# Kernel optimization log

Hardware: AMD Instinct MI355X
Metric: run time of the kernel (lower is better)

The kernel has to match this reference:

```python
import jax, jax.numpy as jnp
import numpy as np
from jax import lax

A = 20          # alphabet size (input_size)
L = 512         # max_seq_length
CH = 8          # conv channels
N_LAYERS = 9    # log2(512) conv+pool stages


def setup_inputs() -> dict:
    key = jax.random.key(0)
    ks = jax.random.split(key, 6)
    B = 1024
    idx = jax.random.randint(ks[0], (B, L), 0, A)
    lens = jax.random.randint(ks[1], (B,), L // 4, L + 1)
    masks = jnp.arange(L)[None, :] < lens[:, None]            # [B, L] bool
    # one-hot sequences, zeroed at padded positions (so nonzero() skips them)
    x = jax.nn.one_hot(idx, A, dtype=jnp.float32) * masks[..., None].astype(jnp.float32)
    blosum = jax.random.normal(ks[2], (A, A), jnp.float32)
    blosum = (blosum + blosum.T) * 0.5                        # symmetric like BLOSUM
    lpm = blosum                                              # trainable copy
    pm = jnp.clip(blosum, 0.0)                                # clamp(min=0) constant
    std = jnp.ones((1,), jnp.float32)                         # Gaussian std for row decay
    w0 = jax.random.normal(ks[3], (CH, 1, 3), jnp.float32) * 0.3
    ws = jax.random.normal(ks[4], (N_LAYERS - 1, CH, CH, 3), jnp.float32) * 0.2
    return {"x": x, "masks": masks, "lpm": lpm, "pm": pm, "std": std, "w0": w0, "ws": ws}


def _shift_pos(m, k):
    # target index clamp(s + k, max=L-1): shift right by k, boundary index L-1
    # collects any source in the last k+1 positions (set semantics -> OR).
    head = jnp.zeros(m.shape[:-1] + (k,), dtype=bool)
    body = m[..., : L - k - 1]                                # targets k .. L-2
    last = jnp.any(m[..., L - 1 - k:], axis=-1, keepdims=True)
    return jnp.concatenate([head, body, last], axis=-1)


def _shift_neg(m, k):
    # target index clamp(s - k, min=0)
    first = jnp.any(m[..., : k + 1], axis=-1, keepdims=True)
    body = m[..., k + 1:]                                     # targets 1 .. L-1-k
    tail = jnp.zeros(m.shape[:-1] + (k,), dtype=bool)
    return jnp.concatenate([first, body, tail], axis=-1)


def _column(nz, lpm, pm):
    # Banded substitution scatter: each one-hot row i writes V[i, r] into row r
    # at the same (batch, seq) position. Original nested index_put loops collapse
    # to a single 20x20 matrix V applied via einsum (one-hot => no collisions).
    ii = jnp.arange(A)[:, None]
    rr = jnp.arange(A)[None, :]
    M = jnp.clip(lpm, 0.001, 1.0) * pm
    # up-writes: j in 1..18-i => i < r <= 18 ; down-writes: j in 1..i => r < i
    V = jnp.where((rr > ii) & (rr <= A - 2), M, 0.0) + jnp.where(rr < ii, M.T, 0.0)
    return jnp.einsum('bis,ir->brs', nz, V)


def _row(m, std):
    # Gaussian positional decay: writes exp(-k^2/(2 std^2)) at seq offsets +-k,
    # k = 1,2,3 in order (later k overwrites earlier at clamp collisions).
    row = jnp.zeros(m.shape, jnp.float32)
    for k in (1, 2, 3):
        mk = _shift_pos(m, k) | _shift_neg(m, k)
        vk = jnp.exp(-(k * k) / (2.0 * std * std))[0]
        row = jnp.where(mk, vk, row)
    return row


def _conv1d(h, w):
    # Conv1d(kernel=3, stride=1, pad=1, no bias)
    return lax.conv_general_dilated(h, w, (1,), [(1, 1)],
                                    dimension_numbers=('NCH', 'OIH', 'NCH'))


def _avgpool2(h):
    N, C, Lh = h.shape
    return h.reshape(N, C, Lh // 2, 2).mean(-1)


def reference(x, masks, lpm, pm, std, w0, ws):
    B = x.shape[0]
    xp = jnp.transpose(x, (0, 2, 1))          # [B, 20, L]
    m = xp != 0
    nz = m.astype(xp.dtype)
    h = xp + _column(nz, lpm, pm) + _row(m, std)
    h = h.reshape(B * A, 1, L)
    h = _avgpool2(_conv1d(h, w0))
    for i in range(N_LAYERS - 1):
        h = _avgpool2(_conv1d(h, ws[i]))
    return h.squeeze(-1).reshape(B, A, -1)    # [B, 20, 8]
```

## Files before the change

kernel.cpp:

```cpp
#include <hip/hip_runtime.h>
#include <math.h>

#define LSEQ 512
#define NA 20
#define NCH 8
#define SV 33
#define PSTRIDE 168

__global__ __launch_bounds__(256) void wf_vt_kernel(
    const float* __restrict__ w0,
    const float* __restrict__ wsg,
    const float* __restrict__ lpm,
    const float* __restrict__ pm,
    float* __restrict__ wf,
    float* __restrict__ vtn)
{
    const int t = threadIdx.x;

    if (blockIdx.x == NCH) {
        for (int o = t; o < NA * NA; o += 256) {
            int j = o / NA, a = o % NA;
            float v = 0.f;
            if (a > j && a <= NA - 2)
                v += fminf(fmaxf(lpm[j * NA + a], 0.001f), 1.0f) * pm[j * NA + a];
            if (a < j)
                v += fminf(fmaxf(lpm[a * NA + j], 0.001f), 1.0f) * pm[a * NA + j];
            vtn[o] = v;
        }
        return;
    }

    const int r = blockIdx.x;

    __shared__ float gA[NCH * 256];
    __shared__ float gB[NCH * 256];
    __shared__ float4 s_e[NCH * NCH];

    if (t < NCH) gA[t * 256] = (t == r) ? 1.f : 0.f;
    __syncthreads();

    int P = 1;
    for (int step = 0; step < 8; ++step) {
        const int li = 7 - step;
        if (t < 64) {
            const int co = t >> 3, ci = t & 7;
            const float* wp = wsg + li * 192 + co * 24 + ci * 3;
            const float a0 = wp[0], a1 = wp[1], a2 = wp[2];
            s_e[co * 8 + ci] = make_float4(a0 + a1, a2, a1 + a2, a0);
        }
        __syncthreads();
        const float* gi = (step & 1) ? gB : gA;
        float* go = (step & 1) ? gA : gB;
        for (int it = t; it < NCH * P; it += 256) {
            const int ci = it >> step;
            const int p = it & (P - 1);
            float accE = 0.f, accO = 0.f;
#pragma unroll
            for (int co = 0; co < NCH; ++co) {
                const float g0 = gi[co * 256 + p];
                const float gm = (p > 0) ? gi[co * 256 + p - 1] : 0.f;
                const float gp = (p + 1 < P) ? gi[co * 256 + p + 1] : 0.f;
                const float4 e = s_e[co * 8 + ci];
                accE += e.x * g0 + e.y * gm;
                accO += e.z * g0 + e.w * gp;
            }
            *(float2*)(go + ci * 256 + 2 * p) = make_float2(0.5f * accE, 0.5f * accO);
        }
        __syncthreads();
        P <<= 1;
    }

    {
        const int p = t;
        float accE = 0.f, accO = 0.f;
#pragma unroll
        for (int co = 0; co < NCH; ++co) {
            const float g0 = gA[co * 256 + p];
            const float gm = (p > 0) ? gA[co * 256 + p - 1] : 0.f;
            const float gp = (p < 255) ? gA[co * 256 + p + 1] : 0.f;
            const float q0 = w0[co * 3 + 0], q1 = w0[co * 3 + 1], q2 = w0[co * 3 + 2];
            accE += (q0 + q1) * g0 + q2 * gm;
            accO += (q1 + q2) * g0 + q0 * gp;
        }
        *(float2*)(wf + r * 512 + 2 * p) = make_float2(0.5f * accE, 0.5f * accO);
    }
}

#define BUILD_H(S_)                                                                     \
    do {                                                                                \
        const int s = (S_);                                                             \
        const int ai = s_idx[s];                                                        \
        const bool valid = ai < NA;                                                     \
        _Pragma("unroll")                                                               \
        for (int a = 0; a < NA; ++a) {                                                  \
            float v = valid ? (s_vtn[ai * SV + a] + (a == ai ? 1.f : 0.f)) : 0.f;       \
            s_h[a * 256 + t] = v;                                                       \
        }                                                                               \
        _Pragma("unroll")                                                               \
        for (int k = 1; k <= 3; ++k) {                                                  \
            const float add = (k == 1) ? vk1 : (k == 2) ? vk2 : vk3;                    \
            if (s == LSEQ - 1) {                                                        \
                for (int u = LSEQ - 1 - k; u <= LSEQ - 1; ++u) {                        \
                    int tg = s_idx[u];                                                  \
                    if (tg < NA)                                                        \
                        s_h[tg * 256 + t] =                                             \
                            (valid ? s_vtn[ai * SV + tg] + (tg == ai ? 1.f : 0.f) : 0.f) + add; \
                }                                                                       \
            } else if (s >= k) {                                                        \
                int tg = s_idx[s - k];                                                  \
                if (tg < NA)                                                            \
                    s_h[tg * 256 + t] =                                                 \
                        (valid ? s_vtn[ai * SV + tg] + (tg == ai ? 1.f : 0.f) : 0.f) + add; \
            }                                                                           \
            if (s == 0) {                                                               \
                for (int u = 0; u <= k; ++u) {                                          \
                    int tg = s_idx[u];                                                  \
                    if (tg < NA)                                                        \
                        s_h[tg * 256 + t] =                                             \
                            (valid ? s_vtn[ai * SV + tg] + (tg == ai ? 1.f : 0.f) : 0.f) + add; \
                }                                                                       \
            } else if (s + k < LSEQ) {                                                  \
                int tg = s_idx[s + k];                                                  \
                if (tg < NA)                                                            \
                    s_h[tg * 256 + t] =                                                 \
                        (valid ? s_vtn[ai * SV + tg] + (tg == ai ? 1.f : 0.f) : 0.f) + add; \
            }                                                                           \
        }                                                                               \
    } while (0)

#define DOT_ROW(J_, ACC_)                                                               \
    do {                                                                                \
        const float4 h = *(const float4*)(s_h + (w5 + (J_)) * 256 + 4 * lane);          \
        float p0 = h.x * wc0.x + h.y * wc0.y + h.z * wc0.z + h.w * wc0.w;               \
        float p1 = h.x * wc1.x + h.y * wc1.y + h.z * wc1.z + h.w * wc1.w;               \
        float p2 = h.x * wc2.x + h.y * wc2.y + h.z * wc2.z + h.w * wc2.w;               \
        float p3 = h.x * wc3.x + h.y * wc3.y + h.z * wc3.z + h.w * wc3.w;               \
        float p4 = h.x * wc4.x + h.y * wc4.y + h.z * wc4.z + h.w * wc4.w;               \
        float p5 = h.x * wc5.x + h.y * wc5.y + h.z * wc5.z + h.w * wc5.w;               \
        float p6 = h.x * wc6.x + h.y * wc6.y + h.z * wc6.z + h.w * wc6.w;               \
        float p7 = h.x * wc7.x + h.y * wc7.y + h.z * wc7.z + h.w * wc7.w;               \
        float r0 = __shfl_xor(b1 ? p0 : p1, 1);                                         \
        float r1 = __shfl_xor(b1 ? p2 : p3, 1);                                         \
        float r2 = __shfl_xor(b1 ? p4 : p5, 1);                                         \
        float r3 = __shfl_xor(b1 ? p6 : p7, 1);                                         \
        float s0 = (b1 ? p1 : p0) + r0;                                                 \
        float s1 = (b1 ? p3 : p2) + r1;                                                 \
        float s2 = (b1 ? p5 : p4) + r2;                                                 \
        float s3 = (b1 ? p7 : p6) + r3;                                                 \
        float v0 = __shfl_xor(b2 ? s0 : s1, 2);                                         \
        float v1 = __shfl_xor(b2 ? s2 : s3, 2);                                         \
        float t0 = (b2 ? s1 : s0) + v0;                                                 \
        float t1 = (b2 ? s3 : s2) + v1;                                                 \
        float rz = __shfl_xor(b4 ? t0 : t1, 4);                                         \
        (ACC_) += (b4 ? t1 : t0) + rz;                                                  \
    } while (0)

#define PHASE2H(HOFF_)                                                                  \
    do {                                                                                \
        const float* wfh = wf + (HOFF_) + 4 * lane;                                     \
        const float4 wc0 = *(const float4*)(wfh + 0 * 512);                             \
        const float4 wc1 = *(const float4*)(wfh + 1 * 512);                             \
        const float4 wc2 = *(const float4*)(wfh + 2 * 512);                             \
        const float4 wc3 = *(const float4*)(wfh + 3 * 512);                             \
        const float4 wc4 = *(const float4*)(wfh + 4 * 512);                             \
        const float4 wc5 = *(const float4*)(wfh + 5 * 512);                             \
        const float4 wc6 = *(const float4*)(wfh + 6 * 512);                             \
        const float4 wc7 = *(const float4*)(wfh + 7 * 512);                             \
        DOT_ROW(0, acc0);                                                               \
        DOT_ROW(1, acc1);                                                               \
        DOT_ROW(2, acc2);                                                               \
        DOT_ROW(3, acc3);                                                               \
        DOT_ROW(4, acc4);                                                               \
    } while (0)

__global__ __launch_bounds__(256, 4) void main_kernel(
    const float* __restrict__ x,
    const float* __restrict__ vtn,
    const float* __restrict__ g_std,
    const float* __restrict__ wf,
    float* __restrict__ out)
{
    const int b = blockIdx.x;
    const int t = threadIdx.x;
    const int w = t >> 6;
    const int lane = t & 63;
    const int w5 = w * 5;

    __shared__ __align__(16) float s_h[NA * 256];
    __shared__ float s_vtn[NA * SV];
    __shared__ float s_part[8 * PSTRIDE];
    __shared__ unsigned char s_idx[LSEQ];

    for (int i = t; i < NA * NA; i += 256) {
        int j = i / NA, a2 = i % NA;
        s_vtn[j * SV + a2] = vtn[i];
    }

    const float4* xb = (const float4*)(x + (size_t)b * LSEQ * NA);
#pragma unroll
    for (int rep = 0; rep < 2; ++rep) {
        int s = t + rep * 256;
        int id = 255;
#pragma unroll
        for (int q = 0; q < 5; ++q) {
            float4 v = xb[s * 5 + q];
            if (v.x > .5f) id = 4 * q + 0;
            if (v.y > .5f) id = 4 * q + 1;
            if (v.z > .5f) id = 4 * q + 2;
            if (v.w > .5f) id = 4 * q + 3;
        }
        s_idx[s] = (unsigned char)id;
    }
    __syncthreads();

    const float stdv = g_std[0];
    const float inv2s2 = 1.f / (2.f * stdv * stdv);
    const float vk1 = __expf(-1.f * inv2s2);
    const float vk2 = __expf(-4.f * inv2s2);
    const float vk3 = __expf(-9.f * inv2s2);

    float acc0 = 0.f, acc1 = 0.f, acc2 = 0.f, acc3 = 0.f, acc4 = 0.f;
    const bool b1 = lane & 1;
    const bool b2 = lane & 2;
    const bool b4 = lane & 4;

    BUILD_H(t);
    __syncthreads();
    PHASE2H(0);
    __syncthreads();

    BUILD_H(256 + t);
    __syncthreads();
    PHASE2H(256);

    {
        const int base = (lane >> 3) * PSTRIDE + (lane & 7);
        s_part[base + (w5 + 0) * 8] = acc0;
        s_part[base + (w5 + 1) * 8] = acc1;
        s_part[base + (w5 + 2) * 8] = acc2;
        s_part[base + (w5 + 3) * 8] = acc3;
        s_part[base + (w5 + 4) * 8] = acc4;
    }
    __syncthreads();

    if (t < NA * NCH)
        out[(size_t)b * (NA * NCH) + t] =
            s_part[0 * PSTRIDE + t] + s_part[1 * PSTRIDE + t]
          + s_part[2 * PSTRIDE + t] + s_part[3 * PSTRIDE + t]
          + s_part[4 * PSTRIDE + t] + s_part[5 * PSTRIDE + t]
          + s_part[6 * PSTRIDE + t] + s_part[7 * PSTRIDE + t];
}

extern "C" void kernel_launch(void* const* d_in, const int* in_sizes, int n_in,
                              void* d_out, int out_size, void* d_ws, size_t ws_size,
                              hipStream_t stream) {
    const float* x    = (const float*)d_in[0];
    const float* lpm  = (const float*)d_in[2];
    const float* pm   = (const float*)d_in[3];
    const float* stdp = (const float*)d_in[4];
    const float* w0   = (const float*)d_in[5];
    const float* wsg  = (const float*)d_in[6];
    float* out = (float*)d_out;

    const int B = in_sizes[0] / (LSEQ * NA);

    float* vtn = (float*)d_ws;
    float* wfb = (float*)d_ws + 1024;

    wf_vt_kernel<<<dim3(NCH + 1), dim3(256), 0, stream>>>(w0, wsg, lpm, pm, wfb, vtn);
    main_kernel<<<dim3(B), dim3(256), 0, stream>>>(x, vtn, stdp, wfb, out);
}
```

Measured before the change: 107.4 us.

## Compute input columns in registers instead of materializing h in shared memory

Removes the shared-memory h buffer and the two build/sync phases. Each lane now derives its four h values per group straight from padded sequence-index bytes, the substitution table and the neighbour-offset decay values, then does the FMA dot products directly. This cuts LDS traffic, shared-memory footprint and barriers, at the cost of more per-element ALU work and recomputing indices for every row. The boundary clamp cases are handled with special lanes.

```diff
diff --git a/kernel.cpp b/kernel.cpp
--- a/kernel.cpp
+++ b/kernel.cpp
@@ -86,59 +86,62 @@
     }
 }
 
-#define BUILD_H(S_)                                                                     \
-    do {                                                                                \
-        const int s = (S_);                                                             \
-        const int ai = s_idx[s];                                                        \
-        const bool valid = ai < NA;                                                     \
-        _Pragma("unroll")                                                               \
-        for (int a = 0; a < NA; ++a) {                                                  \
-            float v = valid ? (s_vtn[ai * SV + a] + (a == ai ? 1.f : 0.f)) : 0.f;       \
-            s_h[a * 256 + t] = v;                                                       \
-        }                                                                               \
-        _Pragma("unroll")                                                               \
-        for (int k = 1; k <= 3; ++k) {                                                  \
-            const float add = (k == 1) ? vk1 : (k == 2) ? vk2 : vk3;                    \
-            if (s == LSEQ - 1) {                                                        \
-                for (int u = LSEQ - 1 - k; u <= LSEQ - 1; ++u) {                        \
-                    int tg = s_idx[u];                                                  \
-                    if (tg < NA)                                                        \
-                        s_h[tg * 256 + t] =                                             \
-                            (valid ? s_vtn[ai * SV + tg] + (tg == ai ? 1.f : 0.f) : 0.f) + add; \
-                }                                                                       \
-            } else if (s >= k) {                                                        \
-                int tg = s_idx[s - k];                                                  \
-                if (tg < NA)                                                            \
-                    s_h[tg * 256 + t] =                                                 \
-                        (valid ? s_vtn[ai * SV + tg] + (tg == ai ? 1.f : 0.f) : 0.f) + add; \
-            }                                                                           \
-            if (s == 0) {                                                               \
-                for (int u = 0; u <= k; ++u) {                                          \
-                    int tg = s_idx[u];                                                  \
-                    if (tg < NA)                                                        \
-                        s_h[tg * 256 + t] =                                             \
-                            (valid ? s_vtn[ai * SV + tg] + (tg == ai ? 1.f : 0.f) : 0.f) + add; \
-                }                                                                       \
-            } else if (s + k < LSEQ) {                                                  \
-                int tg = s_idx[s + k];                                                  \
-                if (tg < NA)                                                            \
-                    s_h[tg * 256 + t] =                                                 \
-                        (valid ? s_vtn[ai * SV + tg] + (tg == ai ? 1.f : 0.f) : 0.f) + add; \
-            }                                                                           \
-        }                                                                               \
-    } while (0)
-
-#define DOT_ROW(J_, ACC_)                                                               \
-    do {                                                                                \
-        const float4 h = *(const float4*)(s_h + (w5 + (J_)) * 256 + 4 * lane);          \
-        float p0 = h.x * wc0.x + h.y * wc0.y + h.z * wc0.z + h.w * wc0.w;               \
-        float p1 = h.x * wc1.x + h.y * wc1.y + h.z * wc1.z + h.w * wc1.w;               \
-        float p2 = h.x * wc2.x + h.y * wc2.y + h.z * wc2.z + h.w * wc2.w;               \
-        float p3 = h.x * wc3.x + h.y * wc3.y + h.z * wc3.z + h.w * wc3.w;               \
-        float p4 = h.x * wc4.x + h.y * wc4.y + h.z * wc4.z + h.w * wc4.w;               \
-        float p5 = h.x * wc5.x + h.y * wc5.y + h.z * wc5.z + h.w * wc5.w;               \
-        float p6 = h.x * wc6.x + h.y * wc6.y + h.z * wc6.z + h.w * wc6.w;               \
-        float p7 = h.x * wc7.x + h.y * wc7.y + h.z * wc7.z + h.w * wc7.w;               \
+#define BYTE_OF(W_, B_) ((int)(((W_) >> ((B_) * 8)) & 255u))
+
+#define COLH(OUT_, AI_, A3_, B3_, A2_, B2_, A1_, B1_, SP_, W4_, W5_, W6_, W7_)          \
+    {                                                                                   \
+        const int ai = (AI_);                                                           \
+        const int aic = ai < NA ? ai : NA - 1;                                          \
+        const float v = s_vtn[aic * SV + a];                                            \
+        const float base = (ai == a) ? v + 1.f : ((ai < NA) ? v : 0.f);                 \
+        const bool h3 = ((A3_) == a) || ((B3_) == a);                                   \
+        const bool h2 = ((A2_) == a) || ((B2_) == a);                                   \
+        const bool h1 = ((A1_) == a) || ((B1_) == a);                                   \
+        float corr = h3 ? vk3 : (h2 ? vk2 : (h1 ? vk1 : 0.f));                          \
+        if ((SP_) == 1 && lane == 0)                                                    \
+            corr = (((W4_) == a) || ((W5_) == a) || ((W6_) == a) || ((W7_) == a))       \
+                       ? vk3 : 0.f;                                                     \
+        if ((SP_) == 2 && lane == 63)                                                   \
+            corr = (((W4_) == a) || ((W5_) == a) || ((W6_) == a) || ((W7_) == a))       \
+                       ? vk3 : 0.f;                                                     \
+        OUT_ = base + corr;                                                             \
+    }
+
+#define GROUP_FMA(G_, B1_, B2_, B3_, B4_, B5_, B6_, B7_, B8_, B9_, B10_)                \
+    {                                                                                   \
+        const float* wfh = wf + (G_)*256 + 4 * lane;                                    \
+        const float4 wc0 = *(const float4*)(wfh + 0 * 512);                             \
+        const float4 wc1 = *(const float4*)(wfh + 1 * 512);                             \
+        const float4 wc2 = *(const float4*)(wfh + 2 * 512);                             \
+        const float4 wc3 = *(const float4*)(wfh + 3 * 512);                             \
+        const float4 wc4 = *(const float4*)(wfh + 4 * 512);                             \
+        const float4 wc5 = *(const float4*)(wfh + 5 * 512);                             \
+        const float4 wc6 = *(const float4*)(wfh + 6 * 512);                             \
+        const float4 wc7 = *(const float4*)(wfh + 7 * 512);                             \
+        float h0, h1v, h2v, h3v;                                                        \
+        COLH(h0,  B4_, B1_, B7_,  B2_, B6_, B3_, B5_, (G_) == 0 ? 1 : 0,                \
+             B4_, B5_, B6_, B7_);                                                       \
+        COLH(h1v, B5_, B2_, B8_,  B3_, B7_, B4_, B6_, 0, 0, 0, 0, 0);                   \
+        COLH(h2v, B6_, B3_, B9_,  B4_, B8_, B5_, B7_, 0, 0, 0, 0, 0);                   \
+        COLH(h3v, B7_, B4_, B10_, B5_, B9_, B6_, B8_, (G_) == 1 ? 2 : 0,                \
+             B4_, B5_, B6_, B7_);                                                       \
+        p0 += h0 * wc0.x + h1v * wc0.y + h2v * wc0.z + h3v * wc0.w;                     \
+        p1 += h0 * wc1.x + h1v * wc1.y + h2v * wc1.z + h3v * wc1.w;                     \
+        p2 += h0 * wc2.x + h1v * wc2.y + h2v * wc2.z + h3v * wc2.w;                     \
+        p3 += h0 * wc3.x + h1v * wc3.y + h2v * wc3.z + h3v * wc3.w;                     \
+        p4 += h0 * wc4.x + h1v * wc4.y + h2v * wc4.z + h3v * wc4.w;                     \
+        p5 += h0 * wc5.x + h1v * wc5.y + h2v * wc5.z + h3v * wc5.w;                     \
+        p6 += h0 * wc6.x + h1v * wc6.y + h2v * wc6.z + h3v * wc6.w;                     \
+        p7 += h0 * wc7.x + h1v * wc7.y + h2v * wc7.z + h3v * wc7.w;                     \
+    }
+
+#define ROW(J_)                                                                         \
+    {                                                                                   \
+        const int a = w5 + (J_);                                                        \
+        float p0 = 0.f, p1 = 0.f, p2 = 0.f, p3 = 0.f;                                   \
+        float p4 = 0.f, p5 = 0.f, p6 = 0.f, p7 = 0.f;                                   \
+        GROUP_FMA(0, a_b1, a_b2, a_b3, a_b4, a_b5, a_b6, a_b7, a_b8, a_b9, a_b10);      \
+        GROUP_FMA(1, c_b1, c_b2, c_b3, c_b4, c_b5, c_b6, c_b7, c_b8, c_b9, c_b10);      \
         float r0 = __shfl_xor(b1 ? p0 : p1, 1);                                         \
         float r1 = __shfl_xor(b1 ? p2 : p3, 1);                                         \
         float r2 = __shfl_xor(b1 ? p4 : p5, 1);                                         \
@@ -152,26 +155,9 @@
         float t0 = (b2 ? s1 : s0) + v0;                                                 \
         float t1 = (b2 ? s3 : s2) + v1;                                                 \
         float rz = __shfl_xor(b4 ? t0 : t1, 4);                                         \
-        (ACC_) += (b4 ? t1 : t0) + rz;                                                  \
-    } while (0)
-
-#define PHASE2H(HOFF_)                                                                  \
-    do {                                                                                \
-        const float* wfh = wf + (HOFF_) + 4 * lane;                                     \
-        const float4 wc0 = *(const float4*)(wfh + 0 * 512);                             \
-        const float4 wc1 = *(const float4*)(wfh + 1 * 512);                             \
-        const float4 wc2 = *(const float4*)(wfh + 2 * 512);                             \
-        const float4 wc3 = *(const float4*)(wfh + 3 * 512);                             \
-        const float4 wc4 = *(const float4*)(wfh + 4 * 512);                             \
-        const float4 wc5 = *(const float4*)(wfh + 5 * 512);                             \
-        const float4 wc6 = *(const float4*)(wfh + 6 * 512);                             \
-        const float4 wc7 = *(const float4*)(wfh + 7 * 512);                             \
-        DOT_ROW(0, acc0);                                                               \
-        DOT_ROW(1, acc1);                                                               \
-        DOT_ROW(2, acc2);                                                               \
-        DOT_ROW(3, acc3);                                                               \
-        DOT_ROW(4, acc4);                                                               \
-    } while (0)
+        float res = (b4 ? t1 : t0) + rz;                                                \
+        s_part[(lane >> 3) * PSTRIDE + a * 8 + (lane & 7)] = res;                       \
+    }
 
 __global__ __launch_bounds__(256, 4) void main_kernel(
     const float* __restrict__ x,
@@ -186,10 +172,9 @@
     const int lane = t & 63;
     const int w5 = w * 5;
 
-    __shared__ __align__(16) float s_h[NA * 256];
     __shared__ float s_vtn[NA * SV];
     __shared__ float s_part[8 * PSTRIDE];
-    __shared__ unsigned char s_idx[LSEQ];
+    __shared__ __align__(4) unsigned char s_eb[520];
 
     for (int i = t; i < NA * NA; i += 256) {
         int j = i / NA, a2 = i % NA;
@@ -209,7 +194,11 @@
             if (v.z > .5f) id = 4 * q + 2;
             if (v.w > .5f) id = 4 * q + 3;
         }
-        s_idx[s] = (unsigned char)id;
+        s_eb[4 + s] = (unsigned char)id;
+    }
+    if (t < 4) {
+        s_eb[t] = 255;
+        s_eb[4 + LSEQ + t] = 255;
     }
     __syncthreads();
 
@@ -219,28 +208,26 @@
     const float vk2 = __expf(-4.f * inv2s2);
     const float vk3 = __expf(-9.f * inv2s2);
 
-    float acc0 = 0.f, acc1 = 0.f, acc2 = 0.f, acc3 = 0.f, acc4 = 0.f;
     const bool b1 = lane & 1;
     const bool b2 = lane & 2;
     const bool b4 = lane & 4;
 
-    BUILD_H(t);
-    __syncthreads();
-    PHASE2H(0);
-    __syncthreads();
-
-    BUILD_H(256 + t);
-    __syncthreads();
-    PHASE2H(256);
-
-    {
-        const int base = (lane >> 3) * PSTRIDE + (lane & 7);
-        s_part[base + (w5 + 0) * 8] = acc0;
-        s_part[base + (w5 + 1) * 8] = acc1;
-        s_part[base + (w5 + 2) * 8] = acc2;
-        s_part[base + (w5 + 3) * 8] = acc3;
-        s_part[base + (w5 + 4) * 8] = acc4;
-    }
+    const unsigned int* ew = (const unsigned int*)s_eb;
+    const unsigned int ga0 = ew[lane], ga1 = ew[lane + 1], ga2 = ew[lane + 2];
+    const unsigned int gc0 = ew[lane + 64], gc1 = ew[lane + 65], gc2 = ew[lane + 66];
+
+    const int a_b1 = BYTE_OF(ga0, 1), a_b2 = BYTE_OF(ga0, 2), a_b3 = BYTE_OF(ga0, 3);
+    const int a_b4 = BYTE_OF(ga1, 0), a_b5 = BYTE_OF(ga1, 1), a_b6 = BYTE_OF(ga1, 2), a_b7 = BYTE_OF(ga1, 3);
+    const int a_b8 = BYTE_OF(ga2, 0), a_b9 = BYTE_OF(ga2, 1), a_b10 = BYTE_OF(ga2, 2);
+    const int c_b1 = BYTE_OF(gc0, 1), c_b2 = BYTE_OF(gc0, 2), c_b3 = BYTE_OF(gc0, 3);
+    const int c_b4 = BYTE_OF(gc1, 0), c_b5 = BYTE_OF(gc1, 1), c_b6 = BYTE_OF(gc1, 2), c_b7 = BYTE_OF(gc1, 3);
+    const int c_b8 = BYTE_OF(gc2, 0), c_b9 = BYTE_OF(gc2, 1), c_b10 = BYTE_OF(gc2, 2);
+
+    ROW(0);
+    ROW(1);
+    ROW(2);
+    ROW(3);
+    ROW(4);
     __syncthreads();
 
     if (t < NA * NCH)
```

Result: no change. 106.5 us (-0.8%).
